# Kernel optimization log

Measured on AMD Instinct MI355X. Metric: run time of the kernel, lower is better.

## Reference

```python
import jax, jax.numpy as jnp
import numpy as np

N, E, H, L, G = 100000, 1000000, 64, 4, 64
D_IN = 2 * H + 3  # edge/coord MLP input: x[row] ++ x[col] ++ rel(3)


def _lin_params(key, fan_in, fan_out):
    kw, kb = jax.random.split(key)
    s = 1.0 / np.sqrt(fan_in)
    w = jax.random.uniform(kw, (fan_in, fan_out), jnp.float32, -s, s)
    b = jax.random.uniform(kb, (fan_out,), jnp.float32, -s, s)
    return w, b


def _stacked(key, fan_in, fan_out, n=L):
    ks = jax.random.split(key, n)
    ws, bs = zip(*[_lin_params(k, fan_in, fan_out) for k in ks])
    return jnp.stack(ws), jnp.stack(bs)


def setup_inputs() -> dict:
    key = jax.random.key(0)
    ks = jax.random.split(key, 16)
    x = jax.random.normal(ks[0], (N, 1), jnp.float32)
    coords = jax.random.normal(ks[1], (N, 3), jnp.float32)
    edge_index = jax.random.randint(ks[2], (2, E), 0, N, jnp.int32)
    batch = jnp.sort(jax.random.randint(ks[3], (N,), 0, G, jnp.int32))
    in_w, in_b = _lin_params(ks[4], 1, H)
    coord_w1, coord_b1 = _stacked(ks[5], D_IN, 2 * H)
    coord_w2, coord_b2 = _stacked(ks[6], 2 * H, 3)
    ew_w, ew_b = _stacked(ks[7], 3, 1)
    cn_scale = jnp.full((L, 1), 0.01, jnp.float32)
    edge_w1, edge_b1 = _stacked(ks[8], D_IN, 2 * H)
    edge_w2, edge_b2 = _stacked(ks[9], 2 * H, H)
    node_w1, node_b1 = _stacked(ks[10], 2 * H, 2 * H)
    node_w2, node_b2 = _stacked(ks[11], 2 * H, H)
    out_w, out_b = _lin_params(ks[12], H, 128)
    return dict(x=x, coords=coords, in_w=in_w, in_b=in_b,
                coord_w1=coord_w1, coord_b1=coord_b1, coord_w2=coord_w2, coord_b2=coord_b2,
                ew_w=ew_w, ew_b=ew_b, cn_scale=cn_scale,
                edge_w1=edge_w1, edge_b1=edge_b1, edge_w2=edge_w2, edge_b2=edge_b2,
                node_w1=node_w1, node_b1=node_b1, node_w2=node_w2, node_b2=node_b2,
                out_w=out_w, out_b=out_b, edge_index=edge_index, batch=batch)


def _layer_norm(h, eps=1e-5):
    mu = jnp.mean(h, -1, keepdims=True)
    var = jnp.var(h, -1, keepdims=True)
    return (h - mu) / jnp.sqrt(var + eps)


def reference(x, coords, in_w, in_b, coord_w1, coord_b1, coord_w2, coord_b2,
              ew_w, ew_b, cn_scale, edge_w1, edge_b1, edge_w2, edge_b2,
              node_w1, node_b1, node_w2, node_b2, out_w, out_b,
              edge_index, batch):
    row, col = edge_index[0], edge_index[1]
    h = x @ in_w + in_b  # [N, H]
    for l in range(L):
        # 1) coord update from OLD coords
        rel = coords[row] - coords[col]                        # [E, 3]
        cin = jnp.concatenate([h[row], h[col], rel], axis=-1)  # [E, 2H+3]
        delta = jax.nn.silu(cin @ coord_w1[l] + coord_b1[l]) @ coord_w2[l] + coord_b2[l]  # [E,3]
        nrm = jnp.maximum(jnp.linalg.norm(delta, axis=-1, keepdims=True), 1e-8)
        delta = delta / nrm * cn_scale[l]                      # CoorsNorm
        delta = delta * jax.nn.sigmoid(rel @ ew_w[l] + ew_b[l])
        coords = coords.at[row].add(delta)
        # 2) edge message / node update from NEW coords
        rel = coords[row] - coords[col]
        ein = jnp.concatenate([h[row], h[col], rel], axis=-1)
        e = jax.nn.silu(jax.nn.silu(ein @ edge_w1[l] + edge_b1[l]) @ edge_w2[l] + edge_b2[l])
        agg = jnp.zeros_like(h).at[row].add(e)                 # scatter-add [N, H]
        nin = jnp.concatenate([h, agg], axis=-1)
        h = h + jax.nn.silu(nin @ node_w1[l] + node_b1[l]) @ node_w2[l] + node_b2[l]
        h = _layer_norm(h)
    # global mean pool
    sums = jax.ops.segment_sum(h, batch, num_segments=G)
    cnts = jax.ops.segment_sum(jnp.ones((h.shape[0], 1), h.dtype), batch, num_segments=G)
    pooled = sums / jnp.maximum(cnts, 1.0)
    out = jax.nn.relu(pooled) @ out_w + out_b                  # [G, 128]
    return out / jnp.maximum(jnp.linalg.norm(out, axis=-1, keepdims=True), 1e-12)
```

## Files before the change

### kernel.cpp

```cpp
#include <hip/hip_runtime.h>
#include <math.h>

#define NN 100000
#define NE 1000000
#define NG 64
#define NL 4
#define NT_E (NE / 32)
#define NT_N (NN / 32)

typedef __attribute__((ext_vector_type(8))) _Float16 f16x8;
typedef __attribute__((ext_vector_type(4))) float f32x4;

#define MFMA16(a, b, c) __builtin_amdgcn_mfma_f32_16x16x32_f16(a, b, c, 0, 0, 0)
#define LOG2E 1.44269504088896340f
__device__ __forceinline__ float fsig_(float x) {
    return __builtin_amdgcn_rcpf(1.0f + __builtin_amdgcn_exp2f(-LOG2E * x));
}
__device__ __forceinline__ float fsilu_(float x) { return x * fsig_(x); }

__global__ void k_init_h(const float* __restrict__ x, const float* __restrict__ in_w,
                         const float* __restrict__ in_b, float* __restrict__ h32,
                         _Float16* __restrict__ h16) {
    int idx = blockIdx.x * blockDim.x + threadIdx.x;
    if (idx >= NN * 64) return;
    int n = idx >> 6, j = idx & 63;
    float v = fmaf(x[n], in_w[j], in_b[j]);
    h32[idx] = v;
    h16[idx] = (_Float16)v;
}

#define SEG0 21504
#define SEG1 21504
#define SEG2 8704
#define SEG3 17408
#define SEG4 8704
#define SEG5 2176
#define SEGTOT (SEG0 + SEG1 + SEG2 + SEG3 + SEG4 + SEG5)
__global__ void k_prep_all(const float* __restrict__ cw1, const float* __restrict__ ew1,
                           const float* __restrict__ ew2, const float* __restrict__ nw1,
                           const float* __restrict__ nw2, const float* __restrict__ cw2,
                           _Float16* __restrict__ cw1T, _Float16* __restrict__ ew1T,
                           _Float16* __restrict__ ew2T, _Float16* __restrict__ nw1T,
                           _Float16* __restrict__ nw2T, _Float16* __restrict__ cw2T) {
    int i = blockIdx.x * blockDim.x + threadIdx.x;
    if (i >= NL * SEGTOT) return;
    int l = i / SEGTOT, r = i - l * SEGTOT;
    const float* src; _Float16* dst; int K, O, SD, j;
    if (r < SEG0) { src = cw1 + (size_t)l * 131 * 128; dst = cw1T + (size_t)l * SEG0; K = 131; O = 128; SD = 168; j = r; }
    else if ((r -= SEG0) < SEG1) { src = ew1 + (size_t)l * 131 * 128; dst = ew1T + (size_t)l * SEG1; K = 131; O = 128; SD = 168; j = r; }
    else if ((r -= SEG1) < SEG2) { src = ew2 + (size_t)l * 128 * 64; dst = ew2T + (size_t)l * SEG2; K = 128; O = 64; SD = 136; j = r; }
    else if ((r -= SEG2) < SEG3) { src = nw1 + (size_t)l * 128 * 128; dst = nw1T + (size_t)l * SEG3; K = 128; O = 128; SD = 136; j = r; }
    else if ((r -= SEG3) < SEG4) { src = nw2 + (size_t)l * 128 * 64; dst = nw2T + (size_t)l * SEG4; K = 128; O = 64; SD = 136; j = r; }
    else {
        r -= SEG4;
        const float* s2 = cw2 + (size_t)l * 128 * 3;
        int o = r / 136, k = r - o * 136;
        cw2T[(size_t)l * SEG5 + r] = (o < 3 && k < 128) ? (_Float16)s2[(size_t)k * 3 + o] : (_Float16)0.0f;
        return;
    }
    int o = j / SD, k = j - o * SD;
    dst[j] = (k < K) ? (_Float16)src[(size_t)k * O + o] : (_Float16)0.0f;
}

__global__ void k_hist(const int* __restrict__ row, int* __restrict__ deg) {
    int e = blockIdx.x * blockDim.x + threadIdx.x;
    if (e < NE) atomicAdd(&deg[row[e]], 1);
}

#define SCB 256
#define SCT 256
#define SCCH ((NN + SCB - 1) / SCB)
__global__ void k_scan_part(const int* __restrict__ deg, int* __restrict__ bsum) {
    __shared__ int red[SCT];
    int b = blockIdx.x;
    int s = b * SCCH, e = min(NN, s + SCCH);
    int sum = 0;
    for (int i = s + threadIdx.x; i < e; i += SCT) sum += deg[i];
    red[threadIdx.x] = sum;
    __syncthreads();
    for (int off = SCT / 2; off > 0; off >>= 1) {
        if (threadIdx.x < off) red[threadIdx.x] += red[threadIdx.x + off];
        __syncthreads();
    }
    if (threadIdx.x == 0) bsum[b] = red[0];
}
__global__ void k_scan_mid(int* __restrict__ bsum) {
    __shared__ int ss[SCB];
    int t = threadIdx.x;
    ss[t] = bsum[t];
    __syncthreads();
    if (t == 0) {
        int run = 0;
        for (int i = 0; i < SCB; ++i) { int v = ss[i]; ss[i] = run; run += v; }
    }
    __syncthreads();
    bsum[t] = ss[t];
}
__global__ void k_scan_fin(const int* __restrict__ deg, const int* __restrict__ bsum,
                           int* __restrict__ rowptr) {
    __shared__ int tsum[SCT];
    int b = blockIdx.x;
    int s = b * SCCH, e = min(NN, s + SCCH);
    const int per = (SCCH + SCT - 1) / SCT;
    int ts = s + threadIdx.x * per;
    int te = min(e, ts + per);
    int sum = 0;
    for (int i = ts; i < te; ++i) sum += deg[i];
    tsum[threadIdx.x] = sum;
    __syncthreads();
    if (threadIdx.x == 0) {
        int run = bsum[b];
        for (int i = 0; i < SCT; ++i) { int v = tsum[i]; tsum[i] = run; run += v; }
    }
    __syncthreads();
    int run = tsum[threadIdx.x];
    for (int i = ts; i < te; ++i) { rowptr[i] = run; run += deg[i]; }
    if (b == 0 && threadIdx.x == 0) rowptr[NN] = NE;
}

__global__ void k_scatter2(const int* __restrict__ row, const int* __restrict__ col,
                           int* __restrict__ pos, int* __restrict__ rowP,
                           int* __restrict__ colP) {
    int e = blockIdx.x * blockDim.x + threadIdx.x;
    if (e < NE) {
        int r = row[e];
        int p = atomicAdd(&pos[r], 1);
        rowP[p] = r;
        colP[p] = col[e];
    }
}

template <int CSR>
__global__ __launch_bounds__(256)
void k_coord3(const _Float16* __restrict__ h16,
              const float* __restrict__ ccur, float* __restrict__ cnext,
              const int* __restrict__ rowP, const int* __restrict__ colP,
              float4* __restrict__ deltas,
              const _Float16* __restrict__ w1T, const float* __restrict__ b1,
              const _Float16* __restrict__ w2T, const float* __restrict__ b2,
              const float* __restrict__ eww, const float* __restrict__ ewb,
              const float* __restrict__ cns) {
    __shared__ __attribute__((aligned(16))) _Float16 cin[32][168];
    __shared__ __attribute__((aligned(16))) _Float16 h1[32][136];
    __shared__ __attribute__((aligned(16))) float pbuf[4][32][17];
    __shared__ float gate[32];
    for (int i = threadIdx.x; i < 32 * 168; i += 256) (&cin[0][0])[i] = (_Float16)0.0f;
    int tid = threadIdx.x;
    int w = tid >> 6, lane = tid & 63, lc = lane & 15, lg = lane >> 4;
    float e0w = eww[0], e1w = eww[1], e2w = eww[2], ebw = ewb[0], sc = cns[0];
    float b20 = b2[0], b21 = b2[1], b22 = b2[2];
    f16x8 bw1[2][5];
#pragma unroll
    for (int ti = 0; ti < 2; ++ti)
#pragma unroll
        for (int ks = 0; ks < 5; ++ks)
            bw1[ti][ks] = *(const f16x8*)&w1T[(size_t)((2 * w + ti) * 16 + lc) * 168 + ks * 32 + lg * 8];
    f16x8 bw2 = *(const f16x8*)&w2T[(size_t)lc * 136 + w * 32 + lg * 8];
    float bias10 = b1[(2 * w) * 16 + lc], bias11 = b1[(2 * w + 1) * 16 + lc];
    __syncthreads();

    for (int tile = blockIdx.x; tile < NT_E; tile += gridDim.x) {
        int e0 = tile * 32;
        {
            int el = tid >> 3, part = tid & 7;
            int r = rowP[e0 + el], c = colP[e0 + el];
            *(f16x8*)&cin[el][part * 8] = *(const f16x8*)&h16[(size_t)r * 64 + part * 8];
            *(f16x8*)&cin[el][64 + part * 8] = *(const f16x8*)&h16[(size_t)c * 64 + part * 8];
        }
        if (tid < 32) {
            int r = rowP[e0 + tid], c = colP[e0 + tid];
            float rx = ccur[r * 3 + 0] - ccur[c * 3 + 0];
            float ry = ccur[r * 3 + 1] - ccur[c * 3 + 1];
            float rz = ccur[r * 3 + 2] - ccur[c * 3 + 2];
            cin[tid][128] = (_Float16)rx; cin[tid][129] = (_Float16)ry; cin[tid][130] = (_Float16)rz;
            gate[tid] = fsig_(fmaf(rx, e0w, fmaf(ry, e1w, fmaf(rz, e2w, ebw))));
        }
        __syncthreads();
        f32x4 acc[2][2];
        acc[0][0] = acc[0][1] = acc[1][0] = acc[1][1] = (f32x4){0.f, 0.f, 0.f, 0.f};
#pragma unroll
        for (int ks = 0; ks < 5; ++ks) {
            f16x8 a0 = *(const f16x8*)&cin[lc][ks * 32 + lg * 8];
            f16x8 a1 = *(const f16x8*)&cin[16 + lc][ks * 32 + lg * 8];
#pragma unroll
            for (int ti = 0; ti < 2; ++ti) {
                acc[0][ti] = MFMA16(a0, bw1[ti][ks], acc[0][ti]);
                acc[1][ti] = MFMA16(a1, bw1[ti][ks], acc[1][ti]);
            }
        }
#pragma unroll
        for (int ti = 0; ti < 2; ++ti) {
            int colc = (2 * w + ti) * 16 + lc;
            float bias = ti ? bias11 : bias10;
#pragma unroll
            for (int rt = 0; rt < 2; ++rt)
#pragma unroll
                for (int j = 0; j < 4; ++j)
                    h1[rt * 16 + lg * 4 + j][colc] = (_Float16)fsilu_(acc[rt][ti][j] + bias);
        }
        __syncthreads();
        f32x4 c2[2];
        c2[0] = c2[1] = (f32x4){0.f, 0.f, 0.f, 0.f};
        {
            f16x8 a0 = *(const f16x8*)&h1[lc][w * 32 + lg * 8];
            f16x8 a1 = *(const f16x8*)&h1[16 + lc][w * 32 + lg * 8];
            c2[0] = MFMA16(a0, bw2, c2[0]);
            c2[1] = MFMA16(a1, bw2, c2[1]);
        }
#pragma unroll
        for (int rt = 0; rt < 2; ++rt)
#pragma unroll
            for (int j = 0; j < 4; ++j)
                pbuf[w][rt * 16 + lg * 4 + j][lc] = c2[rt][j];
        __syncthreads();
        if (tid < 32) {
            float d0 = pbuf[0][tid][0] + pbuf[1][tid][0] + pbuf[2][tid][0] + pbuf[3][tid][0] + b20;
            float d1 = pbuf[0][tid][1] + pbuf[1][tid][1] + pbuf[2][tid][1] + pbuf[3][tid][1] + b21;
            float d2 = pbuf[0][tid][2] + pbuf[1][tid][2] + pbuf[2][tid][2] + pbuf[3][tid][2] + b22;
            float ss = d0 * d0 + d1 * d1 + d2 * d2;
            float nrm = fmaxf(__builtin_amdgcn_sqrtf(ss), 1e-8f);
            float m = sc * __builtin_amdgcn_rcpf(nrm) * gate[tid];
            if (CSR) {
                deltas[e0 + tid] = make_float4(d0 * m, d1 * m, d2 * m, 0.0f);
            } else {
                int r = rowP[e0 + tid];
                atomicAdd(&cnext[(size_t)r * 3 + 0], d0 * m);
                atomicAdd(&cnext[(size_t)r * 3 + 1], d1 * m);
                atomicAdd(&cnext[(size_t)r * 3 + 2], d2 * m);
            }
        }
    }
}

__global__ void k_coord_apply(const float* __restrict__ ccur, float* __restrict__ cnext,
                              const int* __restrict__ rowptr,
                              const float4* __restrict__ deltas) {
    int n = blockIdx.x * blockDim.x + threadIdx.x;
    if (n >= NN) return;
    int s = rowptr[n], e = rowptr[n + 1];
    float d0 = 0.f, d1 = 0.f, d2 = 0.f;
    for (int j = s; j < e; ++j) {
        float4 d = deltas[j];
        d0 += d.x; d1 += d.y; d2 += d.z;
    }
    cnext[(size_t)n * 3 + 0] = ccur[(size_t)n * 3 + 0] + d0;
    cnext[(size_t)n * 3 + 1] = ccur[(size_t)n * 3 + 1] + d1;
    cnext[(size_t)n * 3 + 2] = ccur[(size_t)n * 3 + 2] + d2;
}

template <int CSR>
__global__ __launch_bounds__(256)
void k_edge3(const _Float16* __restrict__ h16, const float* __restrict__ coords,
             float* __restrict__ agg, _Float16* __restrict__ emsgS,
             const int* __restrict__ rowP, const int* __restrict__ colP,
             const _Float16* __restrict__ w1T, const float* __restrict__ b1,
             const _Float16* __restrict__ w2T, const float* __restrict__ b2) {
    __shared__ __attribute__((aligned(16))) _Float16 cin[32][168];
    __shared__ __attribute__((aligned(16))) _Float16 h1[32][136];
    __shared__ __attribute__((aligned(16))) _Float16 msg[32][72];
    for (int i = threadIdx.x; i < 32 * 168; i += 256) (&cin[0][0])[i] = (_Float16)0.0f;
    int tid = threadIdx.x;
    int w = tid >> 6, lane = tid & 63, lc = lane & 15, lg = lane >> 4;
    f16x8 bw1[2][5];
#pragma unroll
    for (int ti = 0; ti < 2; ++ti)
#pragma unroll
        for (int ks = 0; ks < 5; ++ks)
            bw1[ti][ks] = *(const f16x8*)&w1T[(size_t)((2 * w + ti) * 16 + lc) * 168 + ks * 32 + lg * 8];
    f16x8 bw2[4];
#pragma unroll
    for (int ks = 0; ks < 4; ++ks)
        bw2[ks] = *(const f16x8*)&w2T[(size_t)(w * 16 + lc) * 136 + ks * 32 + lg * 8];
    float bias10 = b1[(2 * w) * 16 + lc], bias11 = b1[(2 * w + 1) * 16 + lc];
    float bias2 = b2[w * 16 + lc];
    __syncthreads();

    for (int tile = blockIdx.x; tile < NT_E; tile += gridDim.x) {
        int e0 = tile * 32;
        {
            int el = tid >> 3, part = tid & 7;
            int r = rowP[e0 + el], c = colP[e0 + el];
            *(f16x8*)&cin[el][part * 8] = *(const f16x8*)&h16[(size_t)r * 64 + part * 8];
            *(f16x8*)&cin[el][64 + part * 8] = *(const f16x8*)&h16[(size_t)c * 64 + part * 8];
        }
        if (tid < 32) {
            int r = rowP[e0 + tid], c = colP[e0 + tid];
            cin[tid][128] = (_Float16)(coords[r * 3 + 0] - coords[c * 3 + 0]);
            cin[tid][129] = (_Float16)(coords[r * 3 + 1] - coords[c * 3 + 1]);
            cin[tid][130] = (_Float16)(coords[r * 3 + 2] - coords[c * 3 + 2]);
        }
        __syncthreads();
        f32x4 acc[2][2];
        acc[0][0] = acc[0][1] = acc[1][0] = acc[1][1] = (f32x4){0.f, 0.f, 0.f, 0.f};
#pragma unroll
        for (int ks = 0; ks < 5; ++ks) {
            f16x8 a0 = *(const f16x8*)&cin[lc][ks * 32 + lg * 8];
            f16x8 a1 = *(const f16x8*)&cin[16 + lc][ks * 32 + lg * 8];
#pragma unroll
            for (int ti = 0; ti < 2; ++ti) {
                acc[0][ti] = MFMA16(a0, bw1[ti][ks], acc[0][ti]);
                acc[1][ti] = MFMA16(a1, bw1[ti][ks], acc[1][ti]);
            }
        }
#pragma unroll
        for (int ti = 0; ti < 2; ++ti) {
            int colc = (2 * w + ti) * 16 + lc;
            float bias = ti ? bias11 : bias10;
#pragma unroll
            for (int rt = 0; rt < 2; ++rt)
#pragma unroll
                for (int j = 0; j < 4; ++j)
                    h1[rt * 16 + lg * 4 + j][colc] = (_Float16)fsilu_(acc[rt][ti][j] + bias);
        }
        __syncthreads();
        f32x4 c2[2];
        c2[0] = c2[1] = (f32x4){0.f, 0.f, 0.f, 0.f};
#pragma unroll
        for (int ks = 0; ks < 4; ++ks) {
            f16x8 a0 = *(const f16x8*)&h1[lc][ks * 32 + lg * 8];
            f16x8 a1 = *(const f16x8*)&h1[16 + lc][ks * 32 + lg * 8];
            c2[0] = MFMA16(a0, bw2[ks], c2[0]);
            c2[1] = MFMA16(a1, bw2[ks], c2[1]);
        }
        if (CSR) {
#pragma unroll
            for (int rt = 0; rt < 2; ++rt)
#pragma unroll
                for (int j = 0; j < 4; ++j)
                    msg[rt * 16 + lg * 4 + j][w * 16 + lc] = (_Float16)fsilu_(c2[rt][j] + bias2);
            __syncthreads();
            int r = tid >> 3, part = tid & 7;
            *(f16x8*)&emsgS[(size_t)(e0 + r) * 64 + part * 8] = *(const f16x8*)&msg[r][part * 8];
        } else {
#pragma unroll
            for (int rt = 0; rt < 2; ++rt)
#pragma unroll
                for (int j = 0; j < 4; ++j)
                    atomicAdd(&agg[(size_t)rowP[e0 + rt * 16 + lg * 4 + j] * 64 + w * 16 + lc],
                              fsilu_(c2[rt][j] + bias2));
            __syncthreads();
        }
    }
}

template <int CSR>
__global__ __launch_bounds__(256)
void k_node3(float* __restrict__ h32, _Float16* __restrict__ h16,
             const float* __restrict__ agg, const _Float16* __restrict__ emsgS,
             const int* __restrict__ rowptr,
             const _Float16* __restrict__ w1T, const float* __restrict__ b1,
             const _Float16* __restrict__ w2T, const float* __restrict__ b2) {
    __shared__ __attribute__((aligned(16))) _Float16 cin[32][136];
    __shared__ __attribute__((aligned(16))) _Float16 h1[32][136];
    __shared__ __attribute__((aligned(16))) float vbuf[32][64];
    int tid = threadIdx.x;
    int w = tid >> 6, lane = tid & 63, lc = lane & 15, lg = lane >> 4;
    f16x8 bw1[2][4], bw2[4];
#pragma unroll
    for (int ti = 0; ti < 2; ++ti)
#pragma unroll
        for (int ks = 0; ks < 4; ++ks)
            bw1[ti][ks] = *(const f16x8*)&w1T[(size_t)((2 * w + ti) * 16 + lc) * 136 + ks * 32 + lg * 8];
#pragma unroll
    for (int ks = 0; ks < 4; ++ks)
        bw2[ks] = *(const f16x8*)&w2T[(size_t)(w * 16 + lc) * 136 + ks * 32 + lg * 8];
    float bias10 = b1[(2 * w) * 16 + lc], bias11 = b1[(2 * w + 1) * 16 + lc];
    float bias2 = b2[w * 16 + lc];

    for (int tile = blockIdx.x; tile < NT_N; tile += gridDim.x) {
        int n0 = tile * 32;
        {
            int nl = tid >> 3, part = tid & 7;
            int n = n0 + nl;
            *(f16x8*)&cin[nl][part * 8] = *(const f16x8*)&h16[(size_t)n * 64 + part * 8];
            if (CSR) {
                float a[8] = {0.f, 0.f, 0.f, 0.f, 0.f, 0.f, 0.f, 0.f};
                int s = rowptr[n], e = rowptr[n + 1];
                for (int jj = s; jj < e; ++jj) {
                    f16x8 m = *(const f16x8*)&emsgS[(size_t)jj * 64 + part * 8];
#pragma unroll
                    for (int q = 0; q < 8; ++q) a[q] += (float)m[q];
                }
                f16x8 o;
#pragma unroll
                for (int q = 0; q < 8; ++q) o[q] = (_Float16)a[q];
                *(f16x8*)&cin[nl][64 + part * 8] = o;
            } else {
                f32x4 xx = *(const f32x4*)&agg[(size_t)n * 64 + part * 8];
                f32x4 yy = *(const f32x4*)&agg[(size_t)n * 64 + part * 8 + 4];
                f16x8 o;
                o[0] = (_Float16)xx[0]; o[1] = (_Float16)xx[1]; o[2] = (_Float16)xx[2]; o[3] = (_Float16)xx[3];
                o[4] = (_Float16)yy[0]; o[5] = (_Float16)yy[1]; o[6] = (_Float16)yy[2]; o[7] = (_Float16)yy[3];
                *(f16x8*)&cin[nl][64 + part * 8] = o;
            }
        }
        __syncthreads();
        f32x4 acc[2][2];
        acc[0][0] = acc[0][1] = acc[1][0] = acc[1][1] = (f32x4){0.f, 0.f, 0.f, 0.f};
#pragma unroll
        for (int ks = 0; ks < 4; ++ks) {
            f16x8 a0 = *(const f16x8*)&cin[lc][ks * 32 + lg * 8];
            f16x8 a1 = *(const f16x8*)&cin[16 + lc][ks * 32 + lg * 8];
#pragma unroll
            for (int ti = 0; ti < 2; ++ti) {
                acc[0][ti] = MFMA16(a0, bw1[ti][ks], acc[0][ti]);
                acc[1][ti] = MFMA16(a1, bw1[ti][ks], acc[1][ti]);
            }
        }
#pragma unroll
        for (int ti = 0; ti < 2; ++ti) {
            int colc = (2 * w + ti) * 16 + lc;
            float bias = ti ? bias11 : bias10;
#pragma unroll
            for (int rt = 0; rt < 2; ++rt)
#pragma unroll
                for (int j = 0; j < 4; ++j)
                    h1[rt * 16 + lg * 4 + j][colc] = (_Float16)fsilu_(acc[rt][ti][j] + bias);
        }
        __syncthreads();
        f32x4 c2[2];
        c2[0] = c2[1] = (f32x4){0.f, 0.f, 0.f, 0.f};
#pragma unroll
        for (int ks = 0; ks < 4; ++ks) {
            f16x8 a0 = *(const f16x8*)&h1[lc][ks * 32 + lg * 8];
            f16x8 a1 = *(const f16x8*)&h1[16 + lc][ks * 32 + lg * 8];
            c2[0] = MFMA16(a0, bw2[ks], c2[0]);
            c2[1] = MFMA16(a1, bw2[ks], c2[1]);
        }
#pragma unroll
        for (int rt = 0; rt < 2; ++rt)
#pragma unroll
            for (int j = 0; j < 4; ++j) {
                int rl = rt * 16 + lg * 4 + j, colc = w * 16 + lc;
                vbuf[rl][colc] = h32[(size_t)(n0 + rl) * 64 + colc] + c2[rt][j] + bias2;
            }
        __syncthreads();
        {
            int r = w * 8 + (lane >> 3), sub = lane & 7;
            f32x4 v0 = *(const f32x4*)&vbuf[r][sub * 8];
            f32x4 v1 = *(const f32x4*)&vbuf[r][sub * 8 + 4];
            float s = v0[0] + v0[1] + v0[2] + v0[3] + v1[0] + v1[1] + v1[2] + v1[3];
            float sq = v0[0]*v0[0] + v0[1]*v0[1] + v0[2]*v0[2] + v0[3]*v0[3]
                     + v1[0]*v1[0] + v1[1]*v1[1] + v1[2]*v1[2] + v1[3]*v1[3];
            s += __shfl_xor(s, 1); s += __shfl_xor(s, 2); s += __shfl_xor(s, 4);
            sq += __shfl_xor(sq, 1); sq += __shfl_xor(sq, 2); sq += __shfl_xor(sq, 4);
            float mu = s * (1.0f / 64.0f);
            float var = sq * (1.0f / 64.0f) - mu * mu;
            float rs = __builtin_amdgcn_rcpf(__builtin_amdgcn_sqrtf(var + 1e-5f));
            size_t base = (size_t)(n0 + r) * 64 + sub * 8;
            f32x4 o0, o1; f16x8 oh;
#pragma unroll
            for (int i = 0; i < 4; ++i) {
                o0[i] = (v0[i] - mu) * rs;
                o1[i] = (v1[i] - mu) * rs;
                oh[i] = (_Float16)o0[i];
                oh[4 + i] = (_Float16)o1[i];
            }
            *(f32x4*)&h32[base] = o0;
            *(f32x4*)&h32[base + 4] = o1;
            *(f16x8*)&h16[base] = oh;
        }
        __syncthreads();
    }
}

__global__ void k_pool_seg(const float* __restrict__ h, const int* __restrict__ batch,
                           float* __restrict__ pooled, float* __restrict__ cnt) {
    int lane = threadIdx.x & 63;
    int wid = blockIdx.x * (blockDim.x >> 6) + (threadIdx.x >> 6);
    int nwav = gridDim.x * (blockDim.x >> 6);
    int chunk = (NN + nwav - 1) / nwav;
    int s = wid * chunk;
    if (s >= NN) return;
    int e = s + chunk; if (e > NN) e = NN;
    int g = batch[s];
    float acc = 0.0f, c = 0.0f;
    for (int n = s; n < e; ++n) {
        int b = batch[n];
        if (b != g) {
            atomicAdd(&pooled[g * 64 + lane], acc);
            if (lane == 0) atomicAdd(&cnt[g], c);
            acc = 0.0f; c = 0.0f; g = b;
        }
        acc += h[(size_t)n * 64 + lane];
        c += 1.0f;
    }
    atomicAdd(&pooled[g * 64 + lane], acc);
    if (lane == 0) atomicAdd(&cnt[g], c);
}

__global__ void k_final(const float* __restrict__ pooled, const float* __restrict__ cnt,
                        const float* __restrict__ ow, const float* __restrict__ ob,
                        float* __restrict__ out) {
    __shared__ float red[2];
    int g = blockIdx.x, o = threadIdx.x;
    float c = fmaxf(cnt[g], 1.0f);
    float acc = ob[o];
#pragma unroll
    for (int j = 0; j < 64; ++j) {
        float pm = fmaxf(pooled[g * 64 + j] / c, 0.0f);
        acc = fmaf(pm, ow[j * 128 + o], acc);
    }
    float ss = acc * acc;
#pragma unroll
    for (int off = 32; off > 0; off >>= 1) ss += __shfl_xor(ss, off);
    if ((o & 63) == 0) red[o >> 6] = ss;
    __syncthreads();
    float nrm = sqrtf(red[0] + red[1]);
    out[g * 128 + o] = acc / fmaxf(nrm, 1e-12f);
}

extern "C" void kernel_launch(void* const* d_in, const int* in_sizes, int n_in,
                              void* d_out, int out_size, void* d_ws, size_t ws_size,
                              hipStream_t stream) {
    const float* x         = (const float*)d_in[0];
    const float* coords_in = (const float*)d_in[1];
    const float* in_w      = (const float*)d_in[2];
    const float* in_b      = (const float*)d_in[3];
    const float* coord_w1  = (const float*)d_in[4];
    const float* coord_b1  = (const float*)d_in[5];
    const float* coord_w2  = (const float*)d_in[6];
    const float* coord_b2  = (const float*)d_in[7];
    const float* ew_w      = (const float*)d_in[8];
    const float* ew_b      = (const float*)d_in[9];
    const float* cn_scale  = (const float*)d_in[10];
    const float* edge_w1   = (const float*)d_in[11];
    const float* edge_b1   = (const float*)d_in[12];
    const float* edge_w2   = (const float*)d_in[13];
    const float* edge_b2   = (const float*)d_in[14];
    const float* node_w1   = (const float*)d_in[15];
    const float* node_b1   = (const float*)d_in[16];
    const float* node_w2   = (const float*)d_in[17];
    const float* node_b2   = (const float*)d_in[18];
    const float* out_w     = (const float*)d_in[19];
    const float* out_b     = (const float*)d_in[20];
    const int* ei          = (const int*)d_in[21];
    const int* batch       = (const int*)d_in[22];
    const int* row = ei;
    const int* col = ei + NE;

    char* wp = (char*)d_ws;
    float* h32    = (float*)wp; wp += (size_t)NN * 64 * 4;
    float* cA     = (float*)wp; wp += (size_t)NN * 3 * 4;
    float* cB     = (float*)wp; wp += (size_t)NN * 3 * 4;
    float* pooled = (float*)wp; wp += (size_t)NG * 64 * 4;
    float* cnt    = (float*)wp; wp += (size_t)NG * 4;
    _Float16* h16  = (_Float16*)wp; wp += (size_t)NN * 64 * 2;
    _Float16* cw1T = (_Float16*)wp; wp += (size_t)NL * SEG0 * 2;
    _Float16* ew1T = (_Float16*)wp; wp += (size_t)NL * SEG1 * 2;
    _Float16* ew2T = (_Float16*)wp; wp += (size_t)NL * SEG2 * 2;
    _Float16* nw1T = (_Float16*)wp; wp += (size_t)NL * SEG3 * 2;
    _Float16* nw2T = (_Float16*)wp; wp += (size_t)NL * SEG4 * 2;
    _Float16* cw2T = (_Float16*)wp; wp += (size_t)NL * SEG5 * 2;
    int* deg       = (int*)wp;            wp += (size_t)NN * 4;
    int* rowptr    = (int*)wp;            wp += (size_t)(NN + 4) * 4;
    int* pos       = (int*)wp;            wp += (size_t)NN * 4;
    int* bsum      = (int*)wp;            wp += (size_t)SCB * 4;
    int* rowP      = (int*)wp;            wp += (size_t)NE * 4;
    int* colP      = (int*)wp;            wp += (size_t)NE * 4;
    float4* deltas = (float4*)wp;         wp += (size_t)NE * 16;
    _Float16* emsgS= (_Float16*)wp;       wp += (size_t)NE * 64 * 2;
    size_t csr_need = (size_t)(wp - (char*)d_ws);
    float* agg = (float*)deg;
    bool use_csr = (ws_size >= csr_need);

    if (use_csr) {
        hipMemsetAsync(deg, 0, (size_t)NN * 4, stream);
        k_hist<<<(NE + 255) / 256, 256, 0, stream>>>(row, deg);
        k_scan_part<<<SCB, SCT, 0, stream>>>(deg, bsum);
        k_scan_mid<<<1, SCB, 0, stream>>>(bsum);
        k_scan_fin<<<SCB, SCT, 0, stream>>>(deg, bsum, rowptr);
        hipMemcpyAsync(pos, rowptr, (size_t)NN * 4, hipMemcpyDeviceToDevice, stream);
        k_scatter2<<<(NE + 255) / 256, 256, 0, stream>>>(row, col, pos, rowP, colP);
    }
    k_prep_all<<<(NL * SEGTOT + 255) / 256, 256, 0, stream>>>(
        coord_w1, edge_w1, edge_w2, node_w1, node_w2, coord_w2,
        cw1T, ew1T, ew2T, nw1T, nw2T, cw2T);
    k_init_h<<<(NN * 64 + 255) / 256, 256, 0, stream>>>(x, in_w, in_b, h32, h16);

    const float* cur = coords_in;
    float* nxt = cA;
    for (int l = 0; l < NL; ++l) {
        if (use_csr) {
            k_coord3<1><<<2048, 256, 0, stream>>>(h16, cur, nullptr, rowP, colP, deltas,
                cw1T + (size_t)l * SEG0, coord_b1 + l * 128,
                cw2T + (size_t)l * SEG5, coord_b2 + l * 3,
                ew_w + l * 3, ew_b + l, cn_scale + l);
            k_coord_apply<<<(NN + 255) / 256, 256, 0, stream>>>(cur, nxt, rowptr, deltas);
            k_edge3<1><<<2048, 256, 0, stream>>>(h16, nxt, nullptr, emsgS, rowP, colP,
                ew1T + (size_t)l * SEG1, edge_b1 + l * 128,
                ew2T + (size_t)l * SEG2, edge_b2 + l * 64);
            k_node3<1><<<1024, 256, 0, stream>>>(h32, h16, nullptr, emsgS, rowptr,
                nw1T + (size_t)l * SEG3, node_b1 + l * 128,
                nw2T + (size_t)l * SEG4, node_b2 + l * 64);
        } else {
            hipMemcpyAsync(nxt, cur, (size_t)NN * 3 * sizeof(float), hipMemcpyDeviceToDevice, stream);
            k_coord3<0><<<2048, 256, 0, stream>>>(h16, cur, nxt, row, col, nullptr,
                cw1T + (size_t)l * SEG0, coord_b1 + l * 128,
                cw2T + (size_t)l * SEG5, coord_b2 + l * 3,
                ew_w + l * 3, ew_b + l, cn_scale + l);
            hipMemsetAsync(agg, 0, (size_t)NN * 64 * 4, stream);
            k_edge3<0><<<2048, 256, 0, stream>>>(h16, nxt, agg, nullptr, row, col,
                ew1T + (size_t)l * SEG1, edge_b1 + l * 128,
                ew2T + (size_t)l * SEG2, edge_b2 + l * 64);
            k_node3<0><<<1024, 256, 0, stream>>>(h32, h16, agg, nullptr, nullptr,
                nw1T + (size_t)l * SEG3, node_b1 + l * 128,
                nw2T + (size_t)l * SEG4, node_b2 + l * 64);
        }
        cur = nxt;
        nxt = (nxt == cA) ? cB : cA;
    }
    hipMemsetAsync(pooled, 0, (size_t)(NG * 64 + NG) * sizeof(float), stream);
    k_pool_seg<<<512, 256, 0, stream>>>(h32, batch, pooled, cnt);
    k_final<<<NG, 128, 0, stream>>>(pooled, cnt, out_w, out_b, (float*)d_out);
}
```

Measured before the change: 1.196 ms.

## Permute first-layer weight columns for packed f16x2 LDS stores; drop msg staging and barriers

The first-layer weight output columns are permuted during prep so that each lane's two MFMA output tiles land on adjacent hidden columns. The SiLU results can then be written to LDS as packed f16x2 pairs instead of scalar half stores. The edge kernel now writes messages straight to global memory, dropping the msg shared buffer and its barrier. A trailing barrier is also removed in the node kernel and the atomic path. The direct global stores are scattered 2-byte writes rather than coalesced 16-byte ones, and removing barriers risks LDS reuse hazards across loop iterations.

```diff
diff --git a/kernel.cpp b/kernel.cpp
--- a/kernel.cpp
+++ b/kernel.cpp
@@ -9,6 +9,7 @@
 #define NT_N (NN / 32)
 
 typedef __attribute__((ext_vector_type(8))) _Float16 f16x8;
+typedef __attribute__((ext_vector_type(2))) _Float16 f16x2;
 typedef __attribute__((ext_vector_type(4))) float f32x4;
 
 #define MFMA16(a, b, c) __builtin_amdgcn_mfma_f32_16x16x32_f16(a, b, c, 0, 0, 0)
@@ -45,12 +46,12 @@
     int i = blockIdx.x * blockDim.x + threadIdx.x;
     if (i >= NL * SEGTOT) return;
     int l = i / SEGTOT, r = i - l * SEGTOT;
-    const float* src; _Float16* dst; int K, O, SD, j;
-    if (r < SEG0) { src = cw1 + (size_t)l * 131 * 128; dst = cw1T + (size_t)l * SEG0; K = 131; O = 128; SD = 168; j = r; }
-    else if ((r -= SEG0) < SEG1) { src = ew1 + (size_t)l * 131 * 128; dst = ew1T + (size_t)l * SEG1; K = 131; O = 128; SD = 168; j = r; }
-    else if ((r -= SEG1) < SEG2) { src = ew2 + (size_t)l * 128 * 64; dst = ew2T + (size_t)l * SEG2; K = 128; O = 64; SD = 136; j = r; }
-    else if ((r -= SEG2) < SEG3) { src = nw1 + (size_t)l * 128 * 128; dst = nw1T + (size_t)l * SEG3; K = 128; O = 128; SD = 136; j = r; }
-    else if ((r -= SEG3) < SEG4) { src = nw2 + (size_t)l * 128 * 64; dst = nw2T + (size_t)l * SEG4; K = 128; O = 64; SD = 136; j = r; }
+    const float* src; _Float16* dst; int K, O, SD, j, perm;
+    if (r < SEG0) { src = cw1 + (size_t)l * 131 * 128; dst = cw1T + (size_t)l * SEG0; K = 131; O = 128; SD = 168; j = r; perm = 1; }
+    else if ((r -= SEG0) < SEG1) { src = ew1 + (size_t)l * 131 * 128; dst = ew1T + (size_t)l * SEG1; K = 131; O = 128; SD = 168; j = r; perm = 1; }
+    else if ((r -= SEG1) < SEG2) { src = ew2 + (size_t)l * 128 * 64; dst = ew2T + (size_t)l * SEG2; K = 128; O = 64; SD = 136; j = r; perm = 0; }
+    else if ((r -= SEG2) < SEG3) { src = nw1 + (size_t)l * 128 * 128; dst = nw1T + (size_t)l * SEG3; K = 128; O = 128; SD = 136; j = r; perm = 1; }
+    else if ((r -= SEG3) < SEG4) { src = nw2 + (size_t)l * 128 * 64; dst = nw2T + (size_t)l * SEG4; K = 128; O = 64; SD = 136; j = r; perm = 0; }
     else {
         r -= SEG4;
         const float* s2 = cw2 + (size_t)l * 128 * 3;
@@ -59,14 +60,14 @@
         return;
     }
     int o = j / SD, k = j - o * SD;
-    dst[j] = (k < K) ? (_Float16)src[(size_t)k * O + o] : (_Float16)0.0f;
+    int L = perm ? (32 * (o >> 5) + 2 * (o & 15) + ((o >> 4) & 1)) : o;
+    dst[j] = (k < K) ? (_Float16)src[(size_t)k * O + L] : (_Float16)0.0f;
 }
 
 __global__ void k_hist(const int* __restrict__ row, int* __restrict__ deg) {
     int e = blockIdx.x * blockDim.x + threadIdx.x;
     if (e < NE) atomicAdd(&deg[row[e]], 1);
 }
-
 #define SCB 256
 #define SCT 256
 #define SCCH ((NN + SCB - 1) / SCB)
@@ -117,7 +118,6 @@
     for (int i = ts; i < te; ++i) { rowptr[i] = run; run += deg[i]; }
     if (b == 0 && threadIdx.x == 0) rowptr[NN] = NE;
 }
-
 __global__ void k_scatter2(const int* __restrict__ row, const int* __restrict__ col,
                            int* __restrict__ pos, int* __restrict__ rowP,
                            int* __restrict__ colP) {
@@ -156,7 +156,7 @@
         for (int ks = 0; ks < 5; ++ks)
             bw1[ti][ks] = *(const f16x8*)&w1T[(size_t)((2 * w + ti) * 16 + lc) * 168 + ks * 32 + lg * 8];
     f16x8 bw2 = *(const f16x8*)&w2T[(size_t)lc * 136 + w * 32 + lg * 8];
-    float bias10 = b1[(2 * w) * 16 + lc], bias11 = b1[(2 * w + 1) * 16 + lc];
+    float bias10 = b1[32 * w + 2 * lc], bias11 = b1[32 * w + 2 * lc + 1];
     __syncthreads();
 
     for (int tile = blockIdx.x; tile < NT_E; tile += gridDim.x) {
@@ -189,15 +189,14 @@
             }
         }
 #pragma unroll
-        for (int ti = 0; ti < 2; ++ti) {
-            int colc = (2 * w + ti) * 16 + lc;
-            float bias = ti ? bias11 : bias10;
-#pragma unroll
-            for (int rt = 0; rt < 2; ++rt)
-#pragma unroll
-                for (int j = 0; j < 4; ++j)
-                    h1[rt * 16 + lg * 4 + j][colc] = (_Float16)fsilu_(acc[rt][ti][j] + bias);
-        }
+        for (int rt = 0; rt < 2; ++rt)
+#pragma unroll
+            for (int j = 0; j < 4; ++j) {
+                f16x2 p;
+                p[0] = (_Float16)fsilu_(acc[rt][0][j] + bias10);
+                p[1] = (_Float16)fsilu_(acc[rt][1][j] + bias11);
+                *(f16x2*)&h1[rt * 16 + lg * 4 + j][32 * w + 2 * lc] = p;
+            }
         __syncthreads();
         f32x4 c2[2];
         c2[0] = c2[1] = (f32x4){0.f, 0.f, 0.f, 0.f};
@@ -257,7 +256,6 @@
              const _Float16* __restrict__ w2T, const float* __restrict__ b2) {
     __shared__ __attribute__((aligned(16))) _Float16 cin[32][168];
     __shared__ __attribute__((aligned(16))) _Float16 h1[32][136];
-    __shared__ __attribute__((aligned(16))) _Float16 msg[32][72];
     for (int i = threadIdx.x; i < 32 * 168; i += 256) (&cin[0][0])[i] = (_Float16)0.0f;
     int tid = threadIdx.x;
     int w = tid >> 6, lane = tid & 63, lc = lane & 15, lg = lane >> 4;
@@ -271,7 +269,7 @@
 #pragma unroll
     for (int ks = 0; ks < 4; ++ks)
         bw2[ks] = *(const f16x8*)&w2T[(size_t)(w * 16 + lc) * 136 + ks * 32 + lg * 8];
-    float bias10 = b1[(2 * w) * 16 + lc], bias11 = b1[(2 * w + 1) * 16 + lc];
+    float bias10 = b1[32 * w + 2 * lc], bias11 = b1[32 * w + 2 * lc + 1];
     float bias2 = b2[w * 16 + lc];
     __syncthreads();
 
@@ -303,15 +301,14 @@
             }
         }
 #pragma unroll
-        for (int ti = 0; ti < 2; ++ti) {
-            int colc = (2 * w + ti) * 16 + lc;
-            float bias = ti ? bias11 : bias10;
-#pragma unroll
-            for (int rt = 0; rt < 2; ++rt)
-#pragma unroll
-                for (int j = 0; j < 4; ++j)
-                    h1[rt * 16 + lg * 4 + j][colc] = (_Float16)fsilu_(acc[rt][ti][j] + bias);
-        }
+        for (int rt = 0; rt < 2; ++rt)
+#pragma unroll
+            for (int j = 0; j < 4; ++j) {
+                f16x2 p;
+                p[0] = (_Float16)fsilu_(acc[rt][0][j] + bias10);
+                p[1] = (_Float16)fsilu_(acc[rt][1][j] + bias11);
+                *(f16x2*)&h1[rt * 16 + lg * 4 + j][32 * w + 2 * lc] = p;
+            }
         __syncthreads();
         f32x4 c2[2];
         c2[0] = c2[1] = (f32x4){0.f, 0.f, 0.f, 0.f};
@@ -327,10 +324,8 @@
             for (int rt = 0; rt < 2; ++rt)
 #pragma unroll
                 for (int j = 0; j < 4; ++j)
-                    msg[rt * 16 + lg * 4 + j][w * 16 + lc] = (_Float16)fsilu_(c2[rt][j] + bias2);
-            __syncthreads();
-            int r = tid >> 3, part = tid & 7;
-            *(f16x8*)&emsgS[(size_t)(e0 + r) * 64 + part * 8] = *(const f16x8*)&msg[r][part * 8];
+                    emsgS[(size_t)(e0 + rt * 16 + lg * 4 + j) * 64 + w * 16 + lc] =
+                        (_Float16)fsilu_(c2[rt][j] + bias2);
         } else {
 #pragma unroll
             for (int rt = 0; rt < 2; ++rt)
@@ -338,7 +333,6 @@
                 for (int j = 0; j < 4; ++j)
                     atomicAdd(&agg[(size_t)rowP[e0 + rt * 16 + lg * 4 + j] * 64 + w * 16 + lc],
                               fsilu_(c2[rt][j] + bias2));
-            __syncthreads();
         }
     }
 }
@@ -364,7 +358,7 @@
 #pragma unroll
     for (int ks = 0; ks < 4; ++ks)
         bw2[ks] = *(const f16x8*)&w2T[(size_t)(w * 16 + lc) * 136 + ks * 32 + lg * 8];
-    float bias10 = b1[(2 * w) * 16 + lc], bias11 = b1[(2 * w + 1) * 16 + lc];
+    float bias10 = b1[32 * w + 2 * lc], bias11 = b1[32 * w + 2 * lc + 1];
     float bias2 = b2[w * 16 + lc];
 
     for (int tile = blockIdx.x; tile < NT_N; tile += gridDim.x) {
@@ -408,15 +402,14 @@
             }
         }
 #pragma unroll
-        for (int ti = 0; ti < 2; ++ti) {
-            int colc = (2 * w + ti) * 16 + lc;
-            float bias = ti ? bias11 : bias10;
-#pragma unroll
-            for (int rt = 0; rt < 2; ++rt)
-#pragma unroll
-                for (int j = 0; j < 4; ++j)
-                    h1[rt * 16 + lg * 4 + j][colc] = (_Float16)fsilu_(acc[rt][ti][j] + bias);
-        }
+        for (int rt = 0; rt < 2; ++rt)
+#pragma unroll
+            for (int j = 0; j < 4; ++j) {
+                f16x2 p;
+                p[0] = (_Float16)fsilu_(acc[rt][0][j] + bias10);
+                p[1] = (_Float16)fsilu_(acc[rt][1][j] + bias11);
+                *(f16x2*)&h1[rt * 16 + lg * 4 + j][32 * w + 2 * lc] = p;
+            }
         __syncthreads();
         f32x4 c2[2];
         c2[0] = c2[1] = (f32x4){0.f, 0.f, 0.f, 0.f};
@@ -460,7 +453,6 @@
             *(f32x4*)&h32[base + 4] = o1;
             *(f16x8*)&h16[base] = oh;
         }
-        __syncthreads();
     }
 }
 
```

After: 1.162 ms. -2.8%, faster.
